# Optimization experiments

Measured on AMD Instinct MI355X. Metric: run time of the kernel, lower is better.

## Reference

```python
import jax, jax.numpy as jnp
import numpy as np
import math

B, HQ, HK, M, N, D, S, O, SO = 4, 32, 8, 16, 8192, 128, 256, 8, 64


def _make_proj_score(key):
    # __init__: randn proj, then per-D-column-chunk QR (rot=True), scaled by sqrt(D)
    proj = jax.random.normal(key, (D, S), dtype=jnp.float32)
    chunks = []
    for i in range(0, S, D):
        q, _ = jnp.linalg.qr(proj[:, i:i + D])
        chunks.append(q)
    return (jnp.concatenate(chunks, axis=-1) * math.sqrt(D)).astype(jnp.float32)


def setup_inputs() -> dict:
    key = jax.random.key(0)
    k1, k2, k3, k4 = jax.random.split(key, 4)
    return {
        "query": jax.random.normal(k1, (B, HQ, M, D), dtype=jnp.float32),
        "data": jax.random.normal(k2, (B, HK, N, D), dtype=jnp.float32),
        "proj_dir_score": _make_proj_score(k3),
        "outlier_indices": jax.random.randint(k4, (B, HK, N, O), 0, D, dtype=jnp.int32),
        "dim_outlier": SO,
    }


def reference(query, data, proj_dir_score, outlier_indices, dim_outlier):
    # query: [B,Hq,M,D] fp32; data (keys): [B,Hk,N,D]; proj_dir_score: [D,S]
    Bb, Hk, Nn, Dd = data.shape
    Hq, Mq = query.shape[1], query.shape[2]
    G = Hq // Hk  # GQA repeat factor (repeat_interleave along heads)
    Ss = proj_dir_score.shape[1]
    So = dim_outlier
    dt = data.dtype

    # --- qjl_quant: split keys into inlier / outlier channels per key ---
    # scatter a 0/1 outlier-channel mask: [B,Hk,N,D]
    flat_idx = outlier_indices.reshape(-1, outlier_indices.shape[-1])
    rows = jnp.arange(flat_idx.shape[0])[:, None]
    mask = jnp.zeros((flat_idx.shape[0], Dd), dt).at[rows, flat_idx].set(1.0)
    mask = mask.reshape(Bb, Hk, Nn, Dd)

    k_out = data * mask          # outlier channels only
    k_in = data - k_out          # outlier channels zeroed
    norm_in = jnp.linalg.norm(k_in, axis=-1)    # [B,Hk,N]
    norm_out = jnp.linalg.norm(k_out, axis=-1)  # [B,Hk,N]

    # 1-bit sign-JL quantization (bit-packed in the CUDA kernel; +-1 floats here)
    sign_in = jnp.sign(jnp.einsum('bhnd,ds->bhns', k_in, proj_dir_score))   # [B,Hk,N,S]
    proj_out = proj_dir_score[:, :So]                                       # [D,So]
    sign_out = jnp.sign(jnp.einsum('bhnd,ds->bhns', k_out, proj_out))       # [B,Hk,N,So]

    # --- qjl_gqa_score: QJL unbiased inner-product estimator ---
    # <q,k> ~= sqrt(pi/2)/m * ||k|| * <S q, sign(S k)>, inlier + outlier parts
    coef_in = math.sqrt(math.pi / 2.0) / Ss
    coef_out = math.sqrt(math.pi / 2.0) / So

    k_eff = sign_in * (coef_in * norm_in)[..., None]                        # [B,Hk,N,S]
    # fold outlier part back onto head-dim channels: w_eff[n,d] = mask * (sign_out @ proj_out^T)
    w_eff = mask * jnp.einsum('bhns,ds->bhnd', sign_out, proj_out)
    w_eff = w_eff * (coef_out * norm_out)[..., None]                        # [B,Hk,N,D]

    sketched_q = jnp.einsum('bhmd,ds->bhms', query, proj_dir_score)         # [B,Hq,M,S]
    # group query heads per kv head instead of repeat_interleaving keys (same math)
    sq_g = sketched_q.reshape(Bb, Hk, G, Mq, Ss)
    q_g = query.reshape(Bb, Hk, G, Mq, Dd)

    scores = (jnp.einsum('bhgms,bhns->bhgmn', sq_g, k_eff)
              + jnp.einsum('bhgmd,bhnd->bhgmn', q_g, w_eff))                # [B,Hk,G,M,N]
    scores = scores.reshape(Bb, Hq, Mq, Nn)
    return jnp.swapaxes(scores, -1, -2)  # final .transpose(-1,-2): [B,Hq,N,M]
```

## Files before the change

kernel.cpp:

```cpp
#include <hip/hip_runtime.h>
#include <hip/hip_bf16.h>
#include <math.h>

namespace {
constexpr int B_ = 4, HQ_ = 32, HK_ = 8, G_ = 4, M_ = 16;
constexpr int N_ = 8192, D_ = 128, S_ = 256, O_ = 8;
constexpr int TN = 64;
constexpr float TAU  = 1e-3f;
constexpr float TAUO = 1e-4f;
}

typedef short short8 __attribute__((ext_vector_type(8)));
typedef float f32x4 __attribute__((ext_vector_type(4)));
typedef unsigned int uint4_ __attribute__((ext_vector_type(4)));
typedef unsigned long long ull2 __attribute__((ext_vector_type(2)));

__device__ inline unsigned short f2bf_rne(float f) {
    unsigned u = __float_as_uint(f);
    u += 0x7FFF + ((u >> 16) & 1);
    return (unsigned short)(u >> 16);
}
__device__ inline float bf2f(unsigned short h) {
    return __uint_as_float(((unsigned)h) << 16);
}

__global__ __launch_bounds__(256) void qjl_prept(const float* __restrict__ P,
                                                 unsigned short* __restrict__ PtHi,
                                                 unsigned short* __restrict__ PtLo,
                                                 float* __restrict__ Pt32) {
    const int d = blockIdx.x;
    const int s = threadIdx.x;
    const float f = P[d * S_ + s];
    const unsigned short hb = f2bf_rne(f);
    const float lof = f - bf2f(hb);
    PtHi[s * D_ + d] = hb;
    PtLo[s * D_ + d] = f2bf_rne(lof);
    Pt32[s * D_ + d] = f;
}

__global__ __launch_bounds__(256) void qjl_sketch_q(const float* __restrict__ q,
                                                    const float* __restrict__ P,
                                                    unsigned short* __restrict__ sqHi,
                                                    float* __restrict__ qT) {
    __shared__ float qs[M_][D_];
    const int tid = threadIdx.x;
    const size_t blk = blockIdx.x;
    const float* qb = q + blk * (size_t)(M_ * D_);
    for (int i = tid; i < M_ * D_ / 4; i += 256)
        reinterpret_cast<float4*>(&qs[0][0])[i] = reinterpret_cast<const float4*>(qb)[i];
    __syncthreads();
    float* qtb = qT + blk * (size_t)(D_ * M_);
    for (int i = tid; i < D_ * M_ / 4; i += 256) {
        const int d = i >> 2;
        const int m4 = i & 3;
        float4 v;
        v.x = qs[m4 * 4 + 0][d];
        v.y = qs[m4 * 4 + 1][d];
        v.z = qs[m4 * 4 + 2][d];
        v.w = qs[m4 * 4 + 3][d];
        reinterpret_cast<float4*>(qtb)[i] = v;
    }
    float acc[M_];
#pragma unroll
    for (int m = 0; m < M_; ++m) acc[m] = 0.f;
    const int s = tid;
    for (int d = 0; d < D_; ++d) {
        const float pv = P[d * S_ + s];
#pragma unroll
        for (int m = 0; m < M_; ++m) acc[m] = fmaf(qs[m][d], pv, acc[m]);
    }
    unsigned short* ob = sqHi + blk * (size_t)(M_ * S_);
#pragma unroll
    for (int m = 0; m < M_; ++m) ob[m * S_ + s] = f2bf_rne(acc[m]);
}

__device__ __noinline__ float qjl_fix_coop(const float* __restrict__ drow,
                                           const float* __restrict__ Pt32,
                                           int col, unsigned long long ip,
                                           float a, int src) {
    const int lane = threadIdx.x & 63;
    const float2 dv = *reinterpret_cast<const float2*>(&drow[2 * lane]);
    const float2 pv = *reinterpret_cast<const float2*>(&Pt32[(size_t)col * D_ + 2 * lane]);
    double p = 0.0;
#pragma unroll
    for (int e = 0; e < 2; ++e) {
        const int d = 2 * lane + e;
        const float v = e ? dv.y : dv.x;
        const float pw = e ? pv.y : pv.x;
        bool isout = false;
#pragma unroll
        for (int j = 0; j < 8; ++j)
            isout = isout || (((unsigned)(ip >> (8 * j)) & 0xFFu) == (unsigned)d);
        if (!isout) p = fma((double)v, (double)pw, p);
    }
#pragma unroll
    for (int off = 1; off < 64; off <<= 1) p += __shfl_xor(p, off);
    if (lane == src) a = (p > 0.0) ? 1.f : -1.f;
    return a;
}

__global__ __launch_bounds__(256) void qjl_signs(const float* __restrict__ data,
                                                 const float* __restrict__ P,
                                                 const int* __restrict__ oidx,
                                                 const unsigned short* __restrict__ PtHi,
                                                 const unsigned short* __restrict__ PtLo,
                                                 const float* __restrict__ Pt32,
                                                 unsigned long long* __restrict__ wordsg,
                                                 float* __restrict__ sning,
                                                 float* __restrict__ su2g,
                                                 unsigned long long* __restrict__ sidxpg) {
    __shared__ unsigned short abuf[16384];
    __shared__ unsigned long long sidxp[TN];
    __shared__ float sfull[TN];
    __shared__ float snout[TN];

    const int tid = threadIdx.x;
    const int lane = tid & 63;
    const int wv = tid >> 6;
    const int l15 = lane & 15;
    const int kgrp = (lane >> 4) << 3;
    const int nt = blockIdx.x, hk = blockIdx.y, b = blockIdx.z;
    const int n0 = nt * TN;
    const size_t rowbase = (size_t)(b * HK_ + hk) * N_ + n0;
    const size_t wblk = (size_t)((b * HK_ + hk) * (N_ / TN) + nt);
    const float* dbase = data + ((size_t)(b * HK_ + hk) * N_) * D_;

    {
        const int r = tid >> 2;
        const int c = tid & 3;
        const float* drow = dbase + (size_t)(n0 + r) * D_;
        const int swz = (r & 7) << 3;
        float ssq = 0.f;
#pragma unroll
        for (int k = 0; k < 8; ++k) {
            const int f = c + 4 * k;
            float4 v = reinterpret_cast<const float4*>(drow)[f];
            ssq += v.x * v.x + v.y * v.y + v.z * v.z + v.w * v.w;
            unsigned short h0 = f2bf_rne(v.x), h1 = f2bf_rne(v.y),
                           h2 = f2bf_rne(v.z), h3 = f2bf_rne(v.w);
            unsigned short l0 = f2bf_rne(v.x - bf2f(h0)), l1 = f2bf_rne(v.y - bf2f(h1)),
                           l2 = f2bf_rne(v.z - bf2f(h2)), l3 = f2bf_rne(v.w - bf2f(h3));
            const int ei = r * 128 + ((4 * f) ^ swz);
            unsigned long long hw = (unsigned long long)h0 | ((unsigned long long)h1 << 16) |
                                    ((unsigned long long)h2 << 32) | ((unsigned long long)h3 << 48);
            unsigned long long lw = (unsigned long long)l0 | ((unsigned long long)l1 << 16) |
                                    ((unsigned long long)l2 << 32) | ((unsigned long long)l3 << 48);
            *reinterpret_cast<unsigned long long*>(&abuf[ei]) = hw;
            *reinterpret_cast<unsigned long long*>(&abuf[8192 + ei]) = lw;
        }
        ssq += __shfl_xor(ssq, 1);
        ssq += __shfl_xor(ssq, 2);
        if (c == 0) sfull[r] = ssq;
    }
    __syncthreads();

    if (tid < TN) {
        const int n = tid;
        const int* ob = oidx + ((size_t)(b * HK_ + hk) * N_ + n0 + n) * O_;
        const float* drow = dbase + (size_t)(n0 + n) * D_;
        int id[O_];
        int4 i0 = reinterpret_cast<const int4*>(ob)[0];
        int4 i1 = reinterpret_cast<const int4*>(ob)[1];
        id[0] = i0.x; id[1] = i0.y; id[2] = i0.z; id[3] = i0.w;
        id[4] = i1.x; id[5] = i1.y; id[6] = i1.z; id[7] = i1.w;
        const int swz = (n & 7) << 3;
        unsigned long long ip = 0;
        float so2 = 0.f;
#pragma unroll
        for (int j = 0; j < O_; ++j) {
            bool dup = false;
#pragma unroll
            for (int jj = 0; jj < O_; ++jj)
                if (jj < j) dup = dup || (id[jj] == id[j]);
            if (!dup) {
                const float v = drow[id[j]];
                so2 = fmaf(v, v, so2);
                ip |= (unsigned long long)(id[j] & 0xFF) << (8 * j);
                const int ei = n * 128 + (id[j] ^ swz);
                abuf[ei] = 0;
                abuf[8192 + ei] = 0;
            } else {
                ip |= 0xFFull << (8 * j);
            }
        }
        sidxp[n] = ip;
        sidxpg[rowbase + n] = ip;
        const float CIN = (float)(1.2533141373155003 / 256.0);
        const float COUT = (float)(1.2533141373155003 / 64.0);
        sning[rowbase + n] = CIN * sqrtf(fmaxf(sfull[n] - so2, 0.f));
        snout[n] = COUT * sqrtf(so2);
    }
    __syncthreads();

    {
        const int n = tid >> 2;
        const int c = tid & 3;
        const unsigned long long ip = sidxp[n];
        const float* drow = dbase + (size_t)(n0 + n) * D_;
        float u[O_], vv[O_];
        const float* pr[O_];
        bool val[O_];
#pragma unroll
        for (int j = 0; j < O_; ++j) {
            u[j] = 0.f;
            const unsigned bt = (unsigned)(ip >> (8 * j)) & 0xFFu;
            val[j] = (bt != 0xFFu);
            const int ix = (int)(bt & 0x7Fu);
            pr[j] = P + ix * S_;
            vv[j] = val[j] ? drow[ix] : 0.f;
        }
#pragma unroll
        for (int ch = 0; ch < 4; ++ch) {
            const int tc = c * 16 + ch * 4;
            float4 pj[O_];
#pragma unroll
            for (int j = 0; j < O_; ++j)
                pj[j] = *reinterpret_cast<const float4*>(pr[j] + tc);
#pragma unroll
            for (int e = 0; e < 4; ++e) {
                float cs = 0.f;
#pragma unroll
                for (int j = 0; j < O_; ++j)
                    cs = fmaf(vv[j], pj[j][e], cs);
                float sg;
                if (fabsf(cs) < TAUO) {
                    double cd = 0.0;
#pragma unroll
                    for (int j = 0; j < O_; ++j)
                        cd = fma((double)vv[j], (double)pj[j][e], cd);
                    sg = (cd > 0.0) ? 1.f : ((cd < 0.0) ? -1.f : 0.f);
                } else {
                    sg = (cs > 0.f) ? 1.f : -1.f;
                }
#pragma unroll
                for (int j = 0; j < O_; ++j)
                    u[j] = fmaf(sg, pj[j][e], u[j]);
            }
        }
#pragma unroll
        for (int j = 0; j < O_; ++j) {
            u[j] += __shfl_xor(u[j], 1);
            u[j] += __shfl_xor(u[j], 2);
        }
        if (c == 0) {
            const float cno = snout[n];
            float o[O_];
#pragma unroll
            for (int j = 0; j < O_; ++j) o[j] = val[j] ? u[j] * cno : 0.f;
            float* sp = su2g + (rowbase + n) * O_;
            *reinterpret_cast<f32x4*>(sp) = (f32x4){o[0], o[1], o[2], o[3]};
            *reinterpret_cast<f32x4*>(sp + 4) = (f32x4){o[4], o[5], o[6], o[7]};
        }
    }

    {
        const int t0 = wv * 4;
#pragma unroll
        for (int ti = 0; ti < 4; ++ti) {
            const int t = t0 + ti;
            short8 bhi[4], blo[4];
            const size_t bo = (size_t)(16 * t + l15) * D_ + kgrp;
#pragma unroll
            for (int ks = 0; ks < 4; ++ks) {
                bhi[ks] = *reinterpret_cast<const short8*>(PtHi + bo + ks * 32);
                blo[ks] = *reinterpret_cast<const short8*>(PtLo + bo + ks * 32);
            }
#pragma unroll
            for (int rt = 0; rt < 4; ++rt) {
                const int arow = 16 * rt + l15;
                const int aswz = (arow & 7) << 3;
                short8 ahi[4], alo[4];
#pragma unroll
                for (int ks = 0; ks < 4; ++ks) {
                    const int ei = arow * 128 + ((ks * 32 + kgrp) ^ aswz);
                    ahi[ks] = *reinterpret_cast<const short8*>(&abuf[ei]);
                    alo[ks] = *reinterpret_cast<const short8*>(&abuf[8192 + ei]);
                }
                f32x4 ac1 = (f32x4){0.f, 0.f, 0.f, 0.f};
                f32x4 ac2 = (f32x4){0.f, 0.f, 0.f, 0.f};
                f32x4 ac3 = (f32x4){0.f, 0.f, 0.f, 0.f};
#pragma unroll
                for (int ks = 0; ks < 4; ++ks) {
                    ac1 = __builtin_amdgcn_mfma_f32_16x16x32_bf16(ahi[ks], bhi[ks], ac1, 0, 0, 0);
                    ac2 = __builtin_amdgcn_mfma_f32_16x16x32_bf16(ahi[ks], blo[ks], ac2, 0, 0, 0);
                    ac3 = __builtin_amdgcn_mfma_f32_16x16x32_bf16(alo[ks], bhi[ks], ac3, 0, 0, 0);
                }
                f32x4 a = (ac1 + ac2) + ac3;
                const float mn = fminf(fminf(fabsf(a[0]), fabsf(a[1])),
                                       fminf(fabsf(a[2]), fabsf(a[3])));
                if (__ballot(mn < TAU) != 0ull) {
#pragma unroll
                    for (int r = 0; r < 4; ++r) {
                        unsigned long long low = __ballot(fabsf(a[r]) < TAU);
                        while (low) {
                            const int src = __ffsll((unsigned long long)low) - 1;
                            low &= low - 1;
                            const int row = 16 * rt + ((src >> 4) << 2) + r;
                            const int col = 16 * t + (src & 15);
                            a[r] = qjl_fix_coop(dbase + (size_t)(n0 + row) * D_, Pt32, col,
                                                sidxp[row], a[r], src);
                        }
                    }
                }
                unsigned long long bb0 = __ballot(a[0] > 0.f);
                unsigned long long bb1 = __ballot(a[1] > 0.f);
                unsigned long long bb2 = __ballot(a[2] > 0.f);
                unsigned long long bb3 = __ballot(a[3] > 0.f);
                if (lane == 0) {
                    unsigned long long* wp = wordsg + (wblk * 256 + (size_t)(rt * 16 + t) * 4);
                    *reinterpret_cast<ull2*>(wp) = (ull2){bb0, bb1};
                    *reinterpret_cast<ull2*>(wp + 2) = (ull2){bb2, bb3};
                }
            }
        }
    }
}

__global__ __launch_bounds__(256) void qjl_out(const unsigned short* __restrict__ sqHi,
                                               const float* __restrict__ qT,
                                               const unsigned long long* __restrict__ wordsg,
                                               const float* __restrict__ sning,
                                               const float* __restrict__ su2g,
                                               const unsigned long long* __restrict__ sidxpg,
                                               float* __restrict__ out) {
    __shared__ unsigned short scol[16384];

    const int tid = threadIdx.x;
    const int lane = tid & 63;
    const int wv = tid >> 6;
    const int l15 = lane & 15;
    const int kgrp = (lane >> 4) << 3;
    const int nt = blockIdx.x, hk = blockIdx.y, b = blockIdx.z;
    const int n0 = nt * TN;
    const size_t rowbase = (size_t)(b * HK_ + hk) * N_ + n0;
    const size_t wblk = (size_t)((b * HK_ + hk) * (N_ / TN) + nt);
    const int hq = hk * G_ + wv;

    const unsigned short* sqb = sqHi + (size_t)(b * HQ_ + hq) * (M_ * S_);
    short8 aq[8];
#pragma unroll
    for (int ks = 0; ks < 8; ++ks)
        aq[ks] = *reinterpret_cast<const short8*>(sqb + (size_t)l15 * S_ + ks * 32 + kgrp);

    {
        const int n = tid & 63;
        const int c64 = tid >> 6;
        const unsigned short cb = f2bf_rne(sning[rowbase + n]);
        const unsigned base = (unsigned)cb | ((unsigned)cb << 16);
        const int g = (n >> 2) & 3;
        const int r = n & 3;
        const int w = n >> 4;
        const int swz = (n & 7) << 3;
        const unsigned long long* wbp = wordsg + wblk * 256;
#pragma unroll
        for (int i = 0; i < 4; ++i) {
            const int t = c64 * 4 + i;
            const unsigned long long wd = wbp[(size_t)(w * 16 + t) * 4 + r];
            const unsigned bits = (unsigned)(wd >> (16 * g)) & 0xFFFFu;
            const unsigned nb = ~bits;
            unsigned o[8];
#pragma unroll
            for (int p = 0; p < 8; ++p) {
                const unsigned m = (((nb >> (2 * p)) & 1u) << 15) |
                                   (((nb >> (2 * p + 1)) & 1u) << 31);
                o[p] = base ^ m;
            }
            const int s0 = c64 * 64 + i * 16;
            const int e0 = n * 256 + (s0 ^ swz);
            const int e1 = n * 256 + ((s0 + 8) ^ swz);
            *reinterpret_cast<uint4_*>(&scol[e0]) = (uint4_){o[0], o[1], o[2], o[3]};
            *reinterpret_cast<uint4_*>(&scol[e1]) = (uint4_){o[4], o[5], o[6], o[7]};
        }
    }
    __syncthreads();

    {
        const float* qtb = qT + (size_t)(b * HQ_ + hq) * (D_ * M_);
        const int m0 = (lane >> 4) << 2;
#pragma unroll
        for (int ct = 0; ct < 4; ++ct) {
            const int n = 16 * ct + l15;
            const size_t row = rowbase + n;
            const unsigned long long ip = sidxpg[row];
            const f32x4 s01 = *reinterpret_cast<const f32x4*>(su2g + row * O_);
            const f32x4 s23 = *reinterpret_cast<const f32x4*>(su2g + row * O_ + 4);
            const int nswz = (n & 7) << 3;
            f32x4 acc = (f32x4){0.f, 0.f, 0.f, 0.f};
#pragma unroll
            for (int ks = 0; ks < 8; ++ks) {
                const int ei = n * 256 + ((ks * 32 + kgrp) ^ nswz);
                const short8 bs = *reinterpret_cast<const short8*>(&scol[ei]);
                acc = __builtin_amdgcn_mfma_f32_16x16x32_bf16(aq[ks], bs, acc, 0, 0, 0);
            }
            float a0 = 0.f, a1 = 0.f, a2 = 0.f, a3 = 0.f;
#pragma unroll
            for (int j = 0; j < O_; ++j) {
                const float uj = (j < 4) ? s01[j & 3] : s23[j & 3];
                const int ix = (int)((ip >> (8 * j)) & 0x7Fu);
                const float4 qv = *reinterpret_cast<const float4*>(qtb + ix * M_ + m0);
                a0 = fmaf(uj, qv.x, a0);
                a1 = fmaf(uj, qv.y, a1);
                a2 = fmaf(uj, qv.z, a2);
                a3 = fmaf(uj, qv.w, a3);
            }
            acc[0] += a0; acc[1] += a1; acc[2] += a2; acc[3] += a3;
            float* ob = out + ((size_t)(b * HQ_ + hq) * N_ + (n0 + n)) * M_ + m0;
            *reinterpret_cast<f32x4*>(ob) = acc;
        }
    }
}

extern "C" void kernel_launch(void* const* d_in, const int* in_sizes, int n_in,
                              void* d_out, int out_size, void* d_ws, size_t ws_size,
                              hipStream_t stream) {
    const float* query = (const float*)d_in[0];
    const float* data  = (const float*)d_in[1];
    const float* proj  = (const float*)d_in[2];
    const int*   oidx  = (const int*)d_in[3];

    float* out = (float*)d_out;

    char* ws = (char*)d_ws;
    unsigned short* sqHi  = (unsigned short*)(ws);
    float*          qT    = (float*)(ws + (1 << 20));
    unsigned short* PtHi  = (unsigned short*)(ws + (2 << 20));
    unsigned short* PtLo  = (unsigned short*)(ws + (2 << 20) + (64 << 10));
    float*          Pt32  = (float*)(ws + (2 << 20) + (128 << 10));
    unsigned long long* wordsg = (unsigned long long*)(ws + (3 << 20));
    float*          sning = (float*)(ws + (11 << 20));
    float*          su2g  = (float*)(ws + (12 << 20));
    unsigned long long* sidxpg = (unsigned long long*)(ws + (20 << 20));

    qjl_prept<<<dim3(D_), dim3(S_), 0, stream>>>(proj, PtHi, PtLo, Pt32);
    qjl_sketch_q<<<dim3(B_ * HQ_), dim3(256), 0, stream>>>(query, proj, sqHi, qT);
    qjl_signs<<<dim3(N_ / TN, HK_, B_), dim3(256), 0, stream>>>(
        data, proj, oidx, PtHi, PtLo, Pt32, wordsg, sning, su2g, sidxpg);
    qjl_out<<<dim3(N_ / TN, HK_, B_), dim3(256), 0, stream>>>(
        sqHi, qT, wordsg, sning, su2g, sidxpg, out);
}
```

Measured before the change: 215.0 us.

## Cut register pressure in sign kernel and raise occupancy hints

Adds a min-blocks-per-CU hint of 4 to both kernels and trims live registers in the sign kernel. The outlier loop now uses float2 loads and integer offsets, the A-fragment loads are split into smaller chunks, and the two cross-term MFMA accumulators are merged into one. The bf16 hi/lo split switches from round-to-nearest to truncation with cheaper packing. The aim is more resident waves to hide memory latency, at the cost of possible spills, a slightly different hi/lo error split near the sign threshold, and less reordering freedom for the scheduler.

```diff
diff --git a/kernel.cpp b/kernel.cpp
--- a/kernel.cpp
+++ b/kernel.cpp
@@ -13,6 +13,7 @@
 typedef short short8 __attribute__((ext_vector_type(8)));
 typedef float f32x4 __attribute__((ext_vector_type(4)));
 typedef unsigned int uint4_ __attribute__((ext_vector_type(4)));
+typedef unsigned int uint2_ __attribute__((ext_vector_type(2)));
 typedef unsigned long long ull2 __attribute__((ext_vector_type(2)));
 
 __device__ inline unsigned short f2bf_rne(float f) {
@@ -99,16 +100,16 @@
     return a;
 }
 
-__global__ __launch_bounds__(256) void qjl_signs(const float* __restrict__ data,
-                                                 const float* __restrict__ P,
-                                                 const int* __restrict__ oidx,
-                                                 const unsigned short* __restrict__ PtHi,
-                                                 const unsigned short* __restrict__ PtLo,
-                                                 const float* __restrict__ Pt32,
-                                                 unsigned long long* __restrict__ wordsg,
-                                                 float* __restrict__ sning,
-                                                 float* __restrict__ su2g,
-                                                 unsigned long long* __restrict__ sidxpg) {
+__global__ __launch_bounds__(256, 4) void qjl_signs(const float* __restrict__ data,
+                                                    const float* __restrict__ P,
+                                                    const int* __restrict__ oidx,
+                                                    const unsigned short* __restrict__ PtHi,
+                                                    const unsigned short* __restrict__ PtLo,
+                                                    const float* __restrict__ Pt32,
+                                                    unsigned long long* __restrict__ wordsg,
+                                                    float* __restrict__ sning,
+                                                    float* __restrict__ su2g,
+                                                    unsigned long long* __restrict__ sidxpg) {
     __shared__ unsigned short abuf[16384];
     __shared__ unsigned long long sidxp[TN];
     __shared__ float sfull[TN];
@@ -136,17 +137,19 @@
             const int f = c + 4 * k;
             float4 v = reinterpret_cast<const float4*>(drow)[f];
             ssq += v.x * v.x + v.y * v.y + v.z * v.z + v.w * v.w;
-            unsigned short h0 = f2bf_rne(v.x), h1 = f2bf_rne(v.y),
-                           h2 = f2bf_rne(v.z), h3 = f2bf_rne(v.w);
-            unsigned short l0 = f2bf_rne(v.x - bf2f(h0)), l1 = f2bf_rne(v.y - bf2f(h1)),
-                           l2 = f2bf_rne(v.z - bf2f(h2)), l3 = f2bf_rne(v.w - bf2f(h3));
+            const unsigned u0 = __float_as_uint(v.x), u1 = __float_as_uint(v.y);
+            const unsigned u2 = __float_as_uint(v.z), u3 = __float_as_uint(v.w);
+            const unsigned hw0 = (u0 >> 16) | (u1 & 0xFFFF0000u);
+            const unsigned hw1 = (u2 >> 16) | (u3 & 0xFFFF0000u);
+            const unsigned lu0 = __float_as_uint(v.x - __uint_as_float(u0 & 0xFFFF0000u));
+            const unsigned lu1 = __float_as_uint(v.y - __uint_as_float(u1 & 0xFFFF0000u));
+            const unsigned lu2 = __float_as_uint(v.z - __uint_as_float(u2 & 0xFFFF0000u));
+            const unsigned lu3 = __float_as_uint(v.w - __uint_as_float(u3 & 0xFFFF0000u));
+            const unsigned lw0 = (lu0 >> 16) | (lu1 & 0xFFFF0000u);
+            const unsigned lw1 = (lu2 >> 16) | (lu3 & 0xFFFF0000u);
             const int ei = r * 128 + ((4 * f) ^ swz);
-            unsigned long long hw = (unsigned long long)h0 | ((unsigned long long)h1 << 16) |
-                                    ((unsigned long long)h2 << 32) | ((unsigned long long)h3 << 48);
-            unsigned long long lw = (unsigned long long)l0 | ((unsigned long long)l1 << 16) |
-                                    ((unsigned long long)l2 << 32) | ((unsigned long long)l3 << 48);
-            *reinterpret_cast<unsigned long long*>(&abuf[ei]) = hw;
-            *reinterpret_cast<unsigned long long*>(&abuf[8192 + ei]) = lw;
+            *reinterpret_cast<uint2_*>(&abuf[ei]) = (uint2_){hw0, hw1};
+            *reinterpret_cast<uint2_*>(&abuf[8192 + ei]) = (uint2_){lw0, lw1};
         }
         ssq += __shfl_xor(ssq, 1);
         ssq += __shfl_xor(ssq, 2);
@@ -197,44 +200,42 @@
         const int c = tid & 3;
         const unsigned long long ip = sidxp[n];
         const float* drow = dbase + (size_t)(n0 + n) * D_;
+        int off[O_];
         float u[O_], vv[O_];
-        const float* pr[O_];
-        bool val[O_];
 #pragma unroll
         for (int j = 0; j < O_; ++j) {
             u[j] = 0.f;
             const unsigned bt = (unsigned)(ip >> (8 * j)) & 0xFFu;
-            val[j] = (bt != 0xFFu);
             const int ix = (int)(bt & 0x7Fu);
-            pr[j] = P + ix * S_;
-            vv[j] = val[j] ? drow[ix] : 0.f;
-        }
-#pragma unroll
-        for (int ch = 0; ch < 4; ++ch) {
-            const int tc = c * 16 + ch * 4;
-            float4 pj[O_];
+            off[j] = ix * S_;
+            vv[j] = (bt != 0xFFu) ? drow[ix] : 0.f;
+        }
+#pragma unroll
+        for (int ch = 0; ch < 8; ++ch) {
+            const int tc = c * 16 + ch * 2;
+            float2 pj[O_];
 #pragma unroll
             for (int j = 0; j < O_; ++j)
-                pj[j] = *reinterpret_cast<const float4*>(pr[j] + tc);
-#pragma unroll
-            for (int e = 0; e < 4; ++e) {
+                pj[j] = *reinterpret_cast<const float2*>(P + off[j] + tc);
+#pragma unroll
+            for (int e = 0; e < 2; ++e) {
                 float cs = 0.f;
 #pragma unroll
                 for (int j = 0; j < O_; ++j)
-                    cs = fmaf(vv[j], pj[j][e], cs);
+                    cs = fmaf(vv[j], e ? pj[j].y : pj[j].x, cs);
                 float sg;
                 if (fabsf(cs) < TAUO) {
                     double cd = 0.0;
 #pragma unroll
                     for (int j = 0; j < O_; ++j)
-                        cd = fma((double)vv[j], (double)pj[j][e], cd);
+                        cd = fma((double)vv[j], (double)(e ? pj[j].y : pj[j].x), cd);
                     sg = (cd > 0.0) ? 1.f : ((cd < 0.0) ? -1.f : 0.f);
                 } else {
                     sg = (cs > 0.f) ? 1.f : -1.f;
                 }
 #pragma unroll
                 for (int j = 0; j < O_; ++j)
-                    u[j] = fmaf(sg, pj[j][e], u[j]);
+                    u[j] = fmaf(sg, e ? pj[j].y : pj[j].x, u[j]);
             }
         }
 #pragma unroll
@@ -246,7 +247,8 @@
             const float cno = snout[n];
             float o[O_];
 #pragma unroll
-            for (int j = 0; j < O_; ++j) o[j] = val[j] ? u[j] * cno : 0.f;
+            for (int j = 0; j < O_; ++j)
+                o[j] = (((unsigned)(ip >> (8 * j)) & 0xFFu) != 0xFFu) ? u[j] * cno : 0.f;
             float* sp = su2g + (rowbase + n) * O_;
             *reinterpret_cast<f32x4*>(sp) = (f32x4){o[0], o[1], o[2], o[3]};
             *reinterpret_cast<f32x4*>(sp + 4) = (f32x4){o[4], o[5], o[6], o[7]};
@@ -269,23 +271,27 @@
             for (int rt = 0; rt < 4; ++rt) {
                 const int arow = 16 * rt + l15;
                 const int aswz = (arow & 7) << 3;
-                short8 ahi[4], alo[4];
-#pragma unroll
-                for (int ks = 0; ks < 4; ++ks) {
-                    const int ei = arow * 128 + ((ks * 32 + kgrp) ^ aswz);
-                    ahi[ks] = *reinterpret_cast<const short8*>(&abuf[ei]);
-                    alo[ks] = *reinterpret_cast<const short8*>(&abuf[8192 + ei]);
-                }
                 f32x4 ac1 = (f32x4){0.f, 0.f, 0.f, 0.f};
                 f32x4 ac2 = (f32x4){0.f, 0.f, 0.f, 0.f};
-                f32x4 ac3 = (f32x4){0.f, 0.f, 0.f, 0.f};
-#pragma unroll
-                for (int ks = 0; ks < 4; ++ks) {
-                    ac1 = __builtin_amdgcn_mfma_f32_16x16x32_bf16(ahi[ks], bhi[ks], ac1, 0, 0, 0);
-                    ac2 = __builtin_amdgcn_mfma_f32_16x16x32_bf16(ahi[ks], blo[ks], ac2, 0, 0, 0);
-                    ac3 = __builtin_amdgcn_mfma_f32_16x16x32_bf16(alo[ks], bhi[ks], ac3, 0, 0, 0);
+#pragma unroll
+                for (int kc = 0; kc < 2; ++kc) {
+                    short8 ah[2], al[2];
+#pragma unroll
+                    for (int k2 = 0; k2 < 2; ++k2) {
+                        const int ks = kc * 2 + k2;
+                        const int ei = arow * 128 + ((ks * 32 + kgrp) ^ aswz);
+                        ah[k2] = *reinterpret_cast<const short8*>(&abuf[ei]);
+                        al[k2] = *reinterpret_cast<const short8*>(&abuf[8192 + ei]);
+                    }
+#pragma unroll
+                    for (int k2 = 0; k2 < 2; ++k2) {
+                        const int ks = kc * 2 + k2;
+                        ac1 = __builtin_amdgcn_mfma_f32_16x16x32_bf16(ah[k2], bhi[ks], ac1, 0, 0, 0);
+                        ac2 = __builtin_amdgcn_mfma_f32_16x16x32_bf16(ah[k2], blo[ks], ac2, 0, 0, 0);
+                        ac2 = __builtin_amdgcn_mfma_f32_16x16x32_bf16(al[k2], bhi[ks], ac2, 0, 0, 0);
+                    }
                 }
-                f32x4 a = (ac1 + ac2) + ac3;
+                f32x4 a = ac1 + ac2;
                 const float mn = fminf(fminf(fabsf(a[0]), fabsf(a[1])),
                                        fminf(fabsf(a[2]), fabsf(a[3])));
                 if (__ballot(mn < TAU) != 0ull) {
@@ -316,13 +322,13 @@
     }
 }
 
-__global__ __launch_bounds__(256) void qjl_out(const unsigned short* __restrict__ sqHi,
-                                               const float* __restrict__ qT,
-                                               const unsigned long long* __restrict__ wordsg,
-                                               const float* __restrict__ sning,
-                                               const float* __restrict__ su2g,
-                                               const unsigned long long* __restrict__ sidxpg,
-                                               float* __restrict__ out) {
+__global__ __launch_bounds__(256, 4) void qjl_out(const unsigned short* __restrict__ sqHi,
+                                                  const float* __restrict__ qT,
+                                                  const unsigned long long* __restrict__ wordsg,
+                                                  const float* __restrict__ sning,
+                                                  const float* __restrict__ su2g,
+                                                  const unsigned long long* __restrict__ sidxpg,
+                                                  float* __restrict__ out) {
     __shared__ unsigned short scol[16384];
 
     const int tid = threadIdx.x;
```

Result: slower. 452.3 us (+110.4%).

## Defer sign fixups to a per-wave list and stage sign words in LDS

Applied to the files above, without the earlier changes.

The sign kernel no longer calls a cooperative double-precision fix routine inside the MFMA tile loop. Near-zero projections are recorded in a per-wave shared list (capped at MAXSUS) and fixed after all tiles finish, patching sign words held in LDS. The words are then written to global memory in one coalesced store. Other changes: the bf16 hi/lo split uses truncation instead of round-to-nearest, outlier values are cached in shared memory rather than re-read from global, and qjl_out gets a launch-bounds occupancy hint. The cap on suspects can silently skip fixups when a wave has more than MAXSUS of them.

```diff
diff --git a/kernel.cpp b/kernel.cpp
--- a/kernel.cpp
+++ b/kernel.cpp
@@ -8,12 +8,13 @@
 constexpr int TN = 64;
 constexpr float TAU  = 1e-3f;
 constexpr float TAUO = 1e-4f;
+constexpr int MAXSUS = 32;
 }
 
 typedef short short8 __attribute__((ext_vector_type(8)));
 typedef float f32x4 __attribute__((ext_vector_type(4)));
 typedef unsigned int uint4_ __attribute__((ext_vector_type(4)));
-typedef unsigned long long ull2 __attribute__((ext_vector_type(2)));
+typedef unsigned int uint2_ __attribute__((ext_vector_type(2)));
 
 __device__ inline unsigned short f2bf_rne(float f) {
     unsigned u = __float_as_uint(f);
@@ -74,31 +75,6 @@
     for (int m = 0; m < M_; ++m) ob[m * S_ + s] = f2bf_rne(acc[m]);
 }
 
-__device__ __noinline__ float qjl_fix_coop(const float* __restrict__ drow,
-                                           const float* __restrict__ Pt32,
-                                           int col, unsigned long long ip,
-                                           float a, int src) {
-    const int lane = threadIdx.x & 63;
-    const float2 dv = *reinterpret_cast<const float2*>(&drow[2 * lane]);
-    const float2 pv = *reinterpret_cast<const float2*>(&Pt32[(size_t)col * D_ + 2 * lane]);
-    double p = 0.0;
-#pragma unroll
-    for (int e = 0; e < 2; ++e) {
-        const int d = 2 * lane + e;
-        const float v = e ? dv.y : dv.x;
-        const float pw = e ? pv.y : pv.x;
-        bool isout = false;
-#pragma unroll
-        for (int j = 0; j < 8; ++j)
-            isout = isout || (((unsigned)(ip >> (8 * j)) & 0xFFu) == (unsigned)d);
-        if (!isout) p = fma((double)v, (double)pw, p);
-    }
-#pragma unroll
-    for (int off = 1; off < 64; off <<= 1) p += __shfl_xor(p, off);
-    if (lane == src) a = (p > 0.0) ? 1.f : -1.f;
-    return a;
-}
-
 __global__ __launch_bounds__(256) void qjl_signs(const float* __restrict__ data,
                                                  const float* __restrict__ P,
                                                  const int* __restrict__ oidx,
@@ -110,7 +86,10 @@
                                                  float* __restrict__ su2g,
                                                  unsigned long long* __restrict__ sidxpg) {
     __shared__ unsigned short abuf[16384];
+    __shared__ unsigned long long lwords[256];
+    __shared__ unsigned suslist[4][MAXSUS];
     __shared__ unsigned long long sidxp[TN];
+    __shared__ float svals[TN][O_];
     __shared__ float sfull[TN];
     __shared__ float snout[TN];
 
@@ -136,17 +115,19 @@
             const int f = c + 4 * k;
             float4 v = reinterpret_cast<const float4*>(drow)[f];
             ssq += v.x * v.x + v.y * v.y + v.z * v.z + v.w * v.w;
-            unsigned short h0 = f2bf_rne(v.x), h1 = f2bf_rne(v.y),
-                           h2 = f2bf_rne(v.z), h3 = f2bf_rne(v.w);
-            unsigned short l0 = f2bf_rne(v.x - bf2f(h0)), l1 = f2bf_rne(v.y - bf2f(h1)),
-                           l2 = f2bf_rne(v.z - bf2f(h2)), l3 = f2bf_rne(v.w - bf2f(h3));
+            const unsigned u0 = __float_as_uint(v.x), u1 = __float_as_uint(v.y);
+            const unsigned u2 = __float_as_uint(v.z), u3 = __float_as_uint(v.w);
+            const unsigned hw0 = (u0 >> 16) | (u1 & 0xFFFF0000u);
+            const unsigned hw1 = (u2 >> 16) | (u3 & 0xFFFF0000u);
+            const unsigned lu0 = __float_as_uint(v.x - __uint_as_float(u0 & 0xFFFF0000u));
+            const unsigned lu1 = __float_as_uint(v.y - __uint_as_float(u1 & 0xFFFF0000u));
+            const unsigned lu2 = __float_as_uint(v.z - __uint_as_float(u2 & 0xFFFF0000u));
+            const unsigned lu3 = __float_as_uint(v.w - __uint_as_float(u3 & 0xFFFF0000u));
+            const unsigned lw0 = (lu0 >> 16) | (lu1 & 0xFFFF0000u);
+            const unsigned lw1 = (lu2 >> 16) | (lu3 & 0xFFFF0000u);
             const int ei = r * 128 + ((4 * f) ^ swz);
-            unsigned long long hw = (unsigned long long)h0 | ((unsigned long long)h1 << 16) |
-                                    ((unsigned long long)h2 << 32) | ((unsigned long long)h3 << 48);
-            unsigned long long lw = (unsigned long long)l0 | ((unsigned long long)l1 << 16) |
-                                    ((unsigned long long)l2 << 32) | ((unsigned long long)l3 << 48);
-            *reinterpret_cast<unsigned long long*>(&abuf[ei]) = hw;
-            *reinterpret_cast<unsigned long long*>(&abuf[8192 + ei]) = lw;
+            *reinterpret_cast<uint2_*>(&abuf[ei]) = (uint2_){hw0, hw1};
+            *reinterpret_cast<uint2_*>(&abuf[8192 + ei]) = (uint2_){lw0, lw1};
         }
         ssq += __shfl_xor(ssq, 1);
         ssq += __shfl_xor(ssq, 2);
@@ -175,11 +156,13 @@
             if (!dup) {
                 const float v = drow[id[j]];
                 so2 = fmaf(v, v, so2);
+                svals[n][j] = v;
                 ip |= (unsigned long long)(id[j] & 0xFF) << (8 * j);
                 const int ei = n * 128 + (id[j] ^ swz);
                 abuf[ei] = 0;
                 abuf[8192 + ei] = 0;
             } else {
+                svals[n][j] = 0.f;
                 ip |= 0xFFull << (8 * j);
             }
         }
@@ -196,18 +179,15 @@
         const int n = tid >> 2;
         const int c = tid & 3;
         const unsigned long long ip = sidxp[n];
-        const float* drow = dbase + (size_t)(n0 + n) * D_;
         float u[O_], vv[O_];
         const float* pr[O_];
-        bool val[O_];
 #pragma unroll
         for (int j = 0; j < O_; ++j) {
             u[j] = 0.f;
             const unsigned bt = (unsigned)(ip >> (8 * j)) & 0xFFu;
-            val[j] = (bt != 0xFFu);
             const int ix = (int)(bt & 0x7Fu);
             pr[j] = P + ix * S_;
-            vv[j] = val[j] ? drow[ix] : 0.f;
+            vv[j] = svals[n][j];
         }
 #pragma unroll
         for (int ch = 0; ch < 4; ++ch) {
@@ -246,7 +226,10 @@
             const float cno = snout[n];
             float o[O_];
 #pragma unroll
-            for (int j = 0; j < O_; ++j) o[j] = val[j] ? u[j] * cno : 0.f;
+            for (int j = 0; j < O_; ++j) {
+                const unsigned bt = (unsigned)(ip >> (8 * j)) & 0xFFu;
+                o[j] = (bt != 0xFFu) ? u[j] * cno : 0.f;
+            }
             float* sp = su2g + (rowbase + n) * O_;
             *reinterpret_cast<f32x4*>(sp) = (f32x4){o[0], o[1], o[2], o[3]};
             *reinterpret_cast<f32x4*>(sp + 4) = (f32x4){o[4], o[5], o[6], o[7]};
@@ -254,6 +237,7 @@
     }
 
     {
+        int nsus = 0;
         const int t0 = wv * 4;
 #pragma unroll
         for (int ti = 0; ti < 4; ++ti) {
@@ -286,43 +270,68 @@
                     ac3 = __builtin_amdgcn_mfma_f32_16x16x32_bf16(alo[ks], bhi[ks], ac3, 0, 0, 0);
                 }
                 f32x4 a = (ac1 + ac2) + ac3;
-                const float mn = fminf(fminf(fabsf(a[0]), fabsf(a[1])),
-                                       fminf(fabsf(a[2]), fabsf(a[3])));
-                if (__ballot(mn < TAU) != 0ull) {
-#pragma unroll
-                    for (int r = 0; r < 4; ++r) {
-                        unsigned long long low = __ballot(fabsf(a[r]) < TAU);
-                        while (low) {
-                            const int src = __ffsll((unsigned long long)low) - 1;
-                            low &= low - 1;
-                            const int row = 16 * rt + ((src >> 4) << 2) + r;
-                            const int col = 16 * t + (src & 15);
-                            a[r] = qjl_fix_coop(dbase + (size_t)(n0 + row) * D_, Pt32, col,
-                                                sidxp[row], a[r], src);
+#pragma unroll
+                for (int r = 0; r < 4; ++r) {
+                    const int widx = (rt * 16 + t) * 4 + r;
+                    const unsigned long long bb = __ballot(a[r] > 0.f);
+                    if (lane == 0) lwords[widx] = bb;
+                    unsigned long long low = __ballot(fabsf(a[r]) < TAU);
+                    while (low) {
+                        const int src = __ffsll((unsigned long long)low) - 1;
+                        low &= low - 1;
+                        if (nsus < MAXSUS) {
+                            if (lane == 0)
+                                suslist[wv][nsus] = ((unsigned)widx << 8) | (unsigned)src;
+                            ++nsus;
                         }
                     }
                 }
-                unsigned long long bb0 = __ballot(a[0] > 0.f);
-                unsigned long long bb1 = __ballot(a[1] > 0.f);
-                unsigned long long bb2 = __ballot(a[2] > 0.f);
-                unsigned long long bb3 = __ballot(a[3] > 0.f);
-                if (lane == 0) {
-                    unsigned long long* wp = wordsg + (wblk * 256 + (size_t)(rt * 16 + t) * 4);
-                    *reinterpret_cast<ull2*>(wp) = (ull2){bb0, bb1};
-                    *reinterpret_cast<ull2*>(wp + 2) = (ull2){bb2, bb3};
-                }
-            }
-        }
-    }
-}
-
-__global__ __launch_bounds__(256) void qjl_out(const unsigned short* __restrict__ sqHi,
-                                               const float* __restrict__ qT,
-                                               const unsigned long long* __restrict__ wordsg,
-                                               const float* __restrict__ sning,
-                                               const float* __restrict__ su2g,
-                                               const unsigned long long* __restrict__ sidxpg,
-                                               float* __restrict__ out) {
+            }
+        }
+
+        for (int i = 0; i < nsus; ++i) {
+            const unsigned e = suslist[wv][i];
+            const int widx = (int)(e >> 8), src = (int)(e & 63u);
+            const int t = (widx >> 2) & 15, rt = widx >> 6, r = widx & 3;
+            const int row = 16 * rt + ((src >> 4) << 2) + r;
+            const int col = 16 * t + (src & 15);
+            const float* drow = dbase + (size_t)(n0 + row) * D_;
+            const unsigned long long ip = sidxp[row];
+            const float2 dv = *reinterpret_cast<const float2*>(&drow[2 * lane]);
+            const float2 pv = *reinterpret_cast<const float2*>(&Pt32[(size_t)col * D_ + 2 * lane]);
+            double p = 0.0;
+#pragma unroll
+            for (int ee = 0; ee < 2; ++ee) {
+                const int d = 2 * lane + ee;
+                const float v = ee ? dv.y : dv.x;
+                const float pw = ee ? pv.y : pv.x;
+                bool isout = false;
+#pragma unroll
+                for (int j = 0; j < 8; ++j)
+                    isout = isout || (((unsigned)(ip >> (8 * j)) & 0xFFu) == (unsigned)d);
+                if (!isout) p = fma((double)v, (double)pw, p);
+            }
+#pragma unroll
+            for (int off = 1; off < 64; off <<= 1) p += __shfl_xor(p, off);
+            if (lane == 0) {
+                const unsigned long long bit = 1ull << src;
+                const unsigned long long w = lwords[widx];
+                lwords[widx] = (p > 0.0) ? (w | bit) : (w & ~bit);
+            }
+        }
+
+        const int idx = (lane >> 4) * 64 + wv * 16 + (lane & 15);
+        wordsg[wblk * 256 + idx] = lwords[idx];
+    }
+}
+
+__global__ __launch_bounds__(256, 4) void qjl_out(const unsigned short* __restrict__ sqHi,
+                                                  const float* __restrict__ qT,
+                                                  const unsigned long long* __restrict__ wordsg,
+                                                  const float* __restrict__ sning,
+                                                  const float* __restrict__ su2g,
+                                                  const unsigned long long* __restrict__ sidxpg,
+                                                  float* __restrict__ out) {
     __shared__ unsigned short scol[16384];
 
     const int tid = threadIdx.x;
```

Measured after the change: 223.9 us. 4.2% more time.
